# Kernel optimization log

Measured on AMD Instinct MI355X. Metric: run time of the kernel, lower is better.

Reference implementation:

```python
import jax, jax.numpy as jnp
import numpy as np

B, T, D, F, H = 512, 48, 128, 16, 512


def setup_inputs() -> dict:
    key = jax.random.key(0)
    ks = jax.random.split(key, 7)
    return {
        "input": jax.random.normal(ks[0], (B, T, D, F), dtype=jnp.float32),
        "attn_w": jax.random.normal(ks[1], (2 * H + F * T,), dtype=jnp.float32) * 0.02,
        "attn_b": jax.random.normal(ks[2], (1,), dtype=jnp.float32) * 0.02,
        "w_ih": jax.random.normal(ks[3], (4 * H, D * F), dtype=jnp.float32) * 0.02,
        "w_hh": jax.random.normal(ks[4], (4 * H, H), dtype=jnp.float32) * 0.02,
        "b_ih": jax.random.normal(ks[5], (4 * H,), dtype=jnp.float32) * 0.02,
        "b_hh": jax.random.normal(ks[6], (4 * H,), dtype=jnp.float32) * 0.02,
    }


def reference(input, attn_w, attn_b, w_ih, w_hh, b_ih, b_hh):
    Bsz, Ts, Dn, Fn = input.shape
    Hs = w_hh.shape[1]
    # permute(0,2,3,1): [B, T, D, F] -> [B, D, F, T]
    x_perm = jnp.transpose(input, (0, 2, 3, 1))
    x_flat = x_perm.reshape(Bsz, Dn, Fn * Ts)  # [B, D, F*T]
    # encode_attn input is concat(hidden, cell, x); split the weight accordingly
    w_h, w_c, w_x = attn_w[:Hs], attn_w[Hs:2 * Hs], attn_w[2 * Hs:]
    # x contribution to attention logits is constant across steps
    e_x = x_flat @ w_x + attn_b[0]             # [B, D]
    xs = jnp.moveaxis(x_perm, 3, 0)            # [T, B, D, F] (time-major for scan)
    bias = b_ih + b_hh                         # fuse the two LSTM biases

    def step(carry, x_t):
        h, c = carry                           # [B, H] each
        e = e_x + (h @ w_h)[:, None] + (c @ w_c)[:, None]  # [B, D]
        a = jax.nn.softmax(e, axis=-1)
        x_hat = (a[:, :, None] * x_t).reshape(Bsz, Dn * Fn)  # [B, D*F]
        gates = x_hat @ w_ih.T + h @ w_hh.T + bias            # [B, 4H]
        i, f, g, o = jnp.split(gates, 4, axis=-1)  # torch LSTM gate order
        c_new = jax.nn.sigmoid(f) * c + jax.nn.sigmoid(i) * jnp.tanh(g)
        h_new = jax.nn.sigmoid(o) * jnp.tanh(c_new)
        return (h_new, c_new), h_new

    h0 = jnp.zeros((Bsz, Hs), dtype=input.dtype)
    _, hs = jax.lax.scan(step, (h0, h0), xs)   # hs: [T, B, H]
    return jnp.transpose(hs, (1, 0, 2))        # [B, T, H] == hidden_states[:, 1:]
```

## Files before the change

kernel.cpp:

```cpp
#include <hip/hip_runtime.h>

#define B_ 512
#define T_ 48
#define D_ 128
#define F_ 16
#define H_ 512

typedef float f32x4 __attribute__((ext_vector_type(4)));
typedef short s16x8 __attribute__((ext_vector_type(8)));
typedef unsigned short u16x8 __attribute__((ext_vector_type(8)));
typedef unsigned short u16x4 __attribute__((ext_vector_type(4)));
typedef unsigned long long u64;

__device__ __forceinline__ unsigned short f2bf(float x) {
  unsigned u = __float_as_uint(x);
  u += 0x7fffu + ((u >> 16) & 1u);
  return (unsigned short)(u >> 16);
}
__device__ __forceinline__ float bf2f(unsigned short h) {
  return __uint_as_float(((unsigned)h) << 16);
}
__device__ __forceinline__ float sigmoidf_(float x) {
  return 1.f / (1.f + expf(-x));
}

__device__ __forceinline__ void st_sys_u64(u64* p, u64 v) {
  __hip_atomic_store(p, v, __ATOMIC_RELAXED, __HIP_MEMORY_SCOPE_SYSTEM);
}
__device__ __forceinline__ u64 ld_sys_u64(const u64* p) {
  return __hip_atomic_load((u64*)p, __ATOMIC_RELAXED, __HIP_MEMORY_SCOPE_SYSTEM);
}
__device__ __forceinline__ void st_sys_u32(unsigned* p, unsigned v) {
  __hip_atomic_store(p, v, __ATOMIC_RELAXED, __HIP_MEMORY_SCOPE_SYSTEM);
}
__device__ __forceinline__ unsigned ld_sys_u32(const unsigned* p) {
  return __hip_atomic_load((unsigned*)p, __ATOMIC_RELAXED, __HIP_MEMORY_SCOPE_SYSTEM);
}

#define AS1 __attribute__((address_space(1)))
#define AS3 __attribute__((address_space(3)))
__device__ __forceinline__ void g2lds16(const void* g, void* l) {
  __builtin_amdgcn_global_load_lds((const AS1 void*)g, (AS3 void*)l, 16, 0, 0);
}

__global__ __launch_bounds__(256) void k_prep(const float* __restrict__ wih,
                                              const float* __restrict__ whh,
                                              unsigned short* __restrict__ wih_b,
                                              unsigned short* __restrict__ whh_b) {
  long i4 = ((long)blockIdx.x * 256 + threadIdx.x) * 4;
  if (i4 < 4194304) {
    float4 v = *(const float4*)(wih + i4);
    u16x4 o = {f2bf(v.x), f2bf(v.y), f2bf(v.z), f2bf(v.w)};
    *(u16x4*)(wih_b + i4) = o;
  } else {
    long j = i4 - 4194304;
    if (j < 1048576) {
      float4 v = *(const float4*)(whh + j);
      u16x4 o = {f2bf(v.x), f2bf(v.y), f2bf(v.z), f2bf(v.w)};
      *(u16x4*)(whh_b + j) = o;
    }
  }
}

__global__ __launch_bounds__(128) void k_ex(const float* __restrict__ in,
                                            const float* __restrict__ attn_w,
                                            const float* __restrict__ attn_b,
                                            float* __restrict__ a_out) {
  __shared__ float wx[768];
  __shared__ float red[128];
  const int b = blockIdx.x, d = threadIdx.x;
  for (int i = d; i < 768; i += 128) wx[i] = attn_w[1024 + i];
  __syncthreads();
  const float* base = in + (long)b * 98304 + (long)d * 16;
  float acc = 0.f;
  for (int t = 0; t < 48; ++t) {
    const float4* p = (const float4*)(base + (long)t * 2048);
    float4 v0 = p[0], v1 = p[1], v2 = p[2], v3 = p[3];
    acc += v0.x * wx[t]       + v0.y * wx[48 + t]  + v0.z * wx[96 + t]  + v0.w * wx[144 + t];
    acc += v1.x * wx[192 + t] + v1.y * wx[240 + t] + v1.z * wx[288 + t] + v1.w * wx[336 + t];
    acc += v2.x * wx[384 + t] + v2.y * wx[432 + t] + v2.z * wx[480 + t] + v2.w * wx[528 + t];
    acc += v3.x * wx[576 + t] + v3.y * wx[624 + t] + v3.z * wx[672 + t] + v3.w * wx[720 + t];
  }
  acc += attn_b[0];
  red[d] = acc;
  __syncthreads();
  for (int s = 64; s > 0; s >>= 1) {
    if (d < s) red[d] = fmaxf(red[d], red[d + s]);
    __syncthreads();
  }
  float mx = red[0];
  __syncthreads();
  float ex = expf(acc - mx);
  red[d] = ex;
  __syncthreads();
  for (int s = 64; s > 0; s >>= 1) {
    if (d < s) red[d] += red[d + s];
    __syncthreads();
  }
  a_out[b * 128 + d] = ex / red[0];
}

__global__ __launch_bounds__(256) void k_xhat(const float* __restrict__ in,
                                              const float* __restrict__ a,
                                              unsigned short* __restrict__ xh) {
  const int mrow = blockIdx.x;
  const int t = mrow >> 9, b = mrow & 511;
  const int tid = threadIdx.x;
  const int k = tid * 8;
  const int d = k >> 4;
  const int f0 = k & 15;
  const float* src = in + (((long)(b * 48 + t) * 128 + d) * 16 + f0);
  float4 v0 = *(const float4*)src;
  float4 v1 = *(const float4*)(src + 4);
  float s = a[b * 128 + d];
  u16x8 o;
  o[0] = f2bf(v0.x * s); o[1] = f2bf(v0.y * s); o[2] = f2bf(v0.z * s); o[3] = f2bf(v0.w * s);
  o[4] = f2bf(v1.x * s); o[5] = f2bf(v1.y * s); o[6] = f2bf(v1.z * s); o[7] = f2bf(v1.w * s);
  *(u16x8*)(xh + (long)mrow * 2048 + k) = o;
}


#define G_STAGE(ktv, ksv)                                                       \
  do {                                                                          \
    const long ko_ = (long)(ktv) * 64 + (ksv) * 32;                             \
    char* la_ = (char*)SM + ((ktv) & 1) * 32768 + (ksv) * 16384 + ldsw;         \
    g2lds16(Ag + ko_, la_);                                                     \
    g2lds16(Ag + ko_ + 262144, la_ + 8192);                                     \
    g2lds16(Bg + ko_, la_ + 65536);                                             \
    g2lds16(Bg + ko_ + 262144, la_ + 73728);                                    \
  } while (0)

#define G_LDA(bufel, ksv, mh)                                                   \
  do {                                                                          \
    const unsigned short* ab_ = SM + (bufel) + (ksv) * 8192 + aoff0 + (mh) * 2048; \
    af[0] = *(const s16x8*)(ab_);                                               \
    af[1] = *(const s16x8*)(ab_ + 512);                                         \
    af[2] = *(const s16x8*)(ab_ + 1024);                                        \
    af[3] = *(const s16x8*)(ab_ + 1536);                                        \
  } while (0)

#define G_LDB(bufel, ksv)                                                       \
  do {                                                                          \
    const unsigned short* bb_ = SM + (bufel) + (ksv) * 8192 + boff0;            \
    bv[0] = *(const s16x8*)(bb_);                                               \
    bv[1] = *(const s16x8*)(bb_ + 512);                                         \
    bv[2] = *(const s16x8*)(bb_ + 1024);                                        \
    bv[3] = *(const s16x8*)(bb_ + 1536);                                        \
  } while (0)

#define G_BARW()                                                                \
  do {                                                                          \
    __builtin_amdgcn_s_barrier();                                               \
    asm volatile("s_waitcnt lgkmcnt(0)" ::: "memory");                          \
    __builtin_amdgcn_sched_barrier(0);                                          \
  } while (0)

#define G_MMA(mh)                                                               \
  do {                                                                          \
    __builtin_amdgcn_s_setprio(1);                                              \
    _Pragma("unroll") for (int mt_ = 0; mt_ < 4; ++mt_)                         \
        _Pragma("unroll") for (int nt_ = 0; nt_ < 4; ++nt_)                     \
            acc[(mh) * 4 + mt_][nt_] = __builtin_amdgcn_mfma_f32_16x16x32_bf16( \
                af[mt_], bv[nt_], acc[(mh) * 4 + mt_][nt_], 0, 0, 0);           \
    __builtin_amdgcn_s_setprio(0);                                              \
  } while (0)

#define G_GATE(n) asm volatile("s_waitcnt vmcnt(" #n ")" ::: "memory")

__global__ __launch_bounds__(512, 2) void k_gemm(const unsigned short* __restrict__ A,
                                                 const unsigned short* __restrict__ Bw,
                                                 unsigned short* __restrict__ C) {
  __shared__ __align__(16) unsigned short SM[65536];
  const int tid = threadIdx.x;
  const int w = tid >> 6, lane = tid & 63;
  const int q = lane >> 4, l16 = lane & 15;
  const int wm = w >> 2, wn = w & 3;
  const int id = blockIdx.x;
  const int xcd = id & 7, j = id >> 3;
  const long m0 = ((long)xcd * 12 + (j >> 3)) * 256;
  const long n0 = (long)(j & 7) * 256;

  const int srow = w * 16 + (lane >> 2);
  const int csrc = (lane & 3) ^ ((lane >> 2) & 3);
  const unsigned short* Ag = A + (m0 + srow) * 2048 + csrc * 8;
  const unsigned short* Bg = Bw + (n0 + srow) * 2048 + csrc * 8;
  const int ldsw = w * 1024;

  const int psw = (q ^ (l16 & 3)) * 8;
  const int aoff0 = (wm * 128 + l16) * 32 + psw;
  const int boff0 = 32768 + (wn * 64 + l16) * 32 + psw;

  f32x4 acc[8][4];
  const f32x4 zz = {0.f, 0.f, 0.f, 0.f};
#pragma unroll
  for (int i = 0; i < 8; ++i)
#pragma unroll
    for (int j2 = 0; j2 < 4; ++j2) acc[i][j2] = zz;
  s16x8 af[4], bv[4];

  G_STAGE(0, 0);
  G_STAGE(0, 1);
  G_STAGE(1, 0);
  G_GATE(8);
  __builtin_amdgcn_s_barrier();

#pragma unroll 2
  for (int kt = 0; kt < 30; ++kt) {
    const int bufel = (kt & 1) * 16384;
    G_LDB(bufel, 0); G_LDA(bufel, 0, 0);
    G_STAGE(kt + 1, 1);
    G_BARW(); G_MMA(0);
    __builtin_amdgcn_s_barrier();
    G_LDA(bufel, 0, 1);
    G_BARW(); G_MMA(1);
    G_GATE(8);
    __builtin_amdgcn_s_barrier();
    G_LDB(bufel, 1); G_LDA(bufel, 1, 0);
    G_STAGE(kt + 2, 0);
    G_BARW(); G_MMA(0);
    __builtin_amdgcn_s_barrier();
    G_LDA(bufel, 1, 1);
    G_BARW(); G_MMA(1);
    G_GATE(8);
    __builtin_amdgcn_s_barrier();
  }
  {
    G_LDB(0, 0); G_LDA(0, 0, 0);
    G_STAGE(31, 1);
    G_BARW(); G_MMA(0);
    __builtin_amdgcn_s_barrier();
    G_LDA(0, 0, 1);
    G_BARW(); G_MMA(1);
    G_GATE(8);
    __builtin_amdgcn_s_barrier();
    G_LDB(0, 1); G_LDA(0, 1, 0);
    G_BARW(); G_MMA(0);
    __builtin_amdgcn_s_barrier();
    G_LDA(0, 1, 1);
    G_BARW(); G_MMA(1);
    G_GATE(4);
    __builtin_amdgcn_s_barrier();
  }
  {
    G_LDB(16384, 0); G_LDA(16384, 0, 0);
    G_BARW(); G_MMA(0);
    __builtin_amdgcn_s_barrier();
    G_LDA(16384, 0, 1);
    G_BARW(); G_MMA(1);
    G_GATE(0);
    __builtin_amdgcn_s_barrier();
    G_LDB(16384, 1); G_LDA(16384, 1, 0);
    G_BARW(); G_MMA(0);
    __builtin_amdgcn_s_barrier();
    G_LDA(16384, 1, 1);
    G_BARW(); G_MMA(1);
  }

#pragma unroll
  for (int mh = 0; mh < 2; ++mh)
#pragma unroll
    for (int mt = 0; mt < 4; ++mt)
#pragma unroll
      for (int nt = 0; nt < 4; ++nt)
#pragma unroll
        for (int r = 0; r < 4; ++r) {
          long m = m0 + wm * 128 + mh * 64 + mt * 16 + q * 4 + r;
          long n = n0 + wn * 64 + nt * 16 + l16;
          C[m * 2048 + n] = f2bf(acc[mh * 4 + mt][nt][r]);
        }
}

__global__ __launch_bounds__(256, 1) void k_rec(const unsigned short* __restrict__ gx,
                                                const unsigned short* __restrict__ whh_b,
                                                const float* __restrict__ b_ih,
                                                const float* __restrict__ b_hh,
                                                unsigned short* __restrict__ h_buf,
                                                float* __restrict__ out,
                                                unsigned int* __restrict__ bar) {
  __shared__ unsigned short hs[32 * 528];
  __shared__ float gsm[4 * 32 * 36];
  const int tid = threadIdx.x;
  const int wave = tid >> 6, lane = tid & 63;
  const int q = lane >> 4, l16 = lane & 15;
  const int bt = blockIdx.x & 15, g = blockIdx.x >> 4;
  const int b0 = bt * 32;
  const int pm = tid >> 3, pr = (tid & 7) * 4;
  const int srow = tid >> 3, st7 = tid & 7;
  unsigned int* slots = &bar[bt * 16];

  s16x8 wreg[32];
#pragma unroll
  for (int nt = 0; nt < 2; ++nt) {
    const unsigned short* wp = whh_b + (long)(wave * 512 + g * 32 + nt * 16 + l16) * 512 + q * 8;
#pragma unroll
    for (int kk = 0; kk < 16; ++kk)
      wreg[nt * 16 + kk] = *(const s16x8*)(wp + kk * 32);
  }
#pragma unroll
  for (int i = 0; i < 32; ++i) asm volatile("" : "+v"(wreg[i]));

  float bias_[16];
#pragma unroll
  for (int qq = 0; qq < 4; ++qq)
#pragma unroll
    for (int rr = 0; rr < 4; ++rr) {
      int j = qq * 512 + g * 32 + pr + rr;
      bias_[qq * 4 + rr] = b_ih[j] + b_hh[j];
    }
  float creg[4] = {0.f, 0.f, 0.f, 0.f};
  const f32x4 zz = {0.f, 0.f, 0.f, 0.f};

  for (int t = 0; t < 48; ++t) {
    u16x4 gxr[4];
    const unsigned short* gp = gx + ((long)t * 512 + b0 + pm) * 2048 + g * 32 + pr;
#pragma unroll
    for (int qq = 0; qq < 4; ++qq) gxr[qq] = *(const u16x4*)(gp + qq * 512);

    f32x4 acc[2][2] = {{zz, zz}, {zz, zz}};
    if (t > 0) {
      if (wave == 0 && lane < 16) {
        while (ld_sys_u32(&slots[lane]) < (unsigned)t)
          __builtin_amdgcn_s_sleep(1);
      }
      __syncthreads();
      const u64* hp = (const u64*)(h_buf + ((t - 1) & 1) * (512 * 512) + (long)b0 * 512);
      u64 tmp[16];
#pragma unroll
      for (int j = 0; j < 16; ++j)
        tmp[j] = ld_sys_u64(hp + (long)srow * 128 + st7 + 8 * j);
#pragma unroll
      for (int j = 0; j < 16; ++j)
        *(u64*)&hs[srow * 528 + (st7 + 8 * j) * 4] = tmp[j];
      __syncthreads();
#pragma unroll
      for (int kk = 0; kk < 16; ++kk) {
        s16x8 af0 = *(const s16x8*)&hs[l16 * 528 + kk * 32 + q * 8];
        s16x8 af1 = *(const s16x8*)&hs[(16 + l16) * 528 + kk * 32 + q * 8];
        acc[0][0] = __builtin_amdgcn_mfma_f32_16x16x32_bf16(af0, wreg[kk],      acc[0][0], 0, 0, 0);
        acc[0][1] = __builtin_amdgcn_mfma_f32_16x16x32_bf16(af0, wreg[16 + kk], acc[0][1], 0, 0, 0);
        acc[1][0] = __builtin_amdgcn_mfma_f32_16x16x32_bf16(af1, wreg[kk],      acc[1][0], 0, 0, 0);
        acc[1][1] = __builtin_amdgcn_mfma_f32_16x16x32_bf16(af1, wreg[16 + kk], acc[1][1], 0, 0, 0);
      }
    }
#pragma unroll
    for (int mt = 0; mt < 2; ++mt)
#pragma unroll
      for (int nt = 0; nt < 2; ++nt)
        *(f32x4*)&gsm[(wave * 32 + nt * 16 + l16) * 36 + mt * 16 + q * 4] = acc[mt][nt];
    __syncthreads();
    float hval[4];
#pragma unroll
    for (int rr = 0; rr < 4; ++rr) {
      float gv[4];
#pragma unroll
      for (int qq = 0; qq < 4; ++qq)
        gv[qq] = gsm[(qq * 32 + pr + rr) * 36 + pm] + bf2f(gxr[qq][rr]) + bias_[qq * 4 + rr];
      float is = sigmoidf_(gv[0]);
      float fs = sigmoidf_(gv[1]);
      float gt = tanhf(gv[2]);
      float os = sigmoidf_(gv[3]);
      creg[rr] = fs * creg[rr] + is * gt;
      hval[rr] = os * tanhf(creg[rr]);
    }
    u16x4 hb = {f2bf(hval[0]), f2bf(hval[1]), f2bf(hval[2]), f2bf(hval[3])};
    u64 hb8;
    __builtin_memcpy(&hb8, &hb, 8);
    st_sys_u64((u64*)&h_buf[(t & 1) * (512 * 512) + (b0 + pm) * 512 + g * 32 + pr], hb8);
    f32x4 ov = {hval[0], hval[1], hval[2], hval[3]};
    __builtin_nontemporal_store(ov, (f32x4*)&out[(long)(b0 + pm) * (T_ * H_) + (long)t * H_ + g * 32 + pr]);
    __syncthreads();
    if (t < 47 && tid == 0)
      st_sys_u32(&slots[g], (unsigned)(t + 1));
  }
}

extern "C" void kernel_launch(void* const* d_in, const int* in_sizes, int n_in,
                              void* d_out, int out_size, void* d_ws, size_t ws_size,
                              hipStream_t stream) {
  const float* input  = (const float*)d_in[0];
  const float* attn_w = (const float*)d_in[1];
  const float* attn_b = (const float*)d_in[2];
  const float* w_ih   = (const float*)d_in[3];
  const float* w_hh   = (const float*)d_in[4];
  const float* b_ih   = (const float*)d_in[5];
  const float* b_hh   = (const float*)d_in[6];
  float* out = (float*)d_out;

  char* ws = (char*)d_ws;
  unsigned int* bar     = (unsigned int*)ws;
  float* a_ws           = (float*)(ws + 1024);
  unsigned short* h_buf = (unsigned short*)(ws + 263168);
  unsigned short* whh_b = (unsigned short*)(ws + 1311744);
  unsigned short* wih_b = (unsigned short*)(ws + 3408896);
  unsigned short* x_hat = (unsigned short*)(ws + 11797504);
  unsigned short* gxws  = (unsigned short*)(ws + 112460800);

  (void)hipMemsetAsync(d_ws, 0, 1024, stream);
  hipLaunchKernelGGL(k_prep, dim3(5120), dim3(256), 0, stream, w_ih, w_hh, wih_b, whh_b);
  hipLaunchKernelGGL(k_ex, dim3(512), dim3(128), 0, stream, input, attn_w, attn_b, a_ws);
  hipLaunchKernelGGL(k_xhat, dim3(24576), dim3(256), 0, stream, input, a_ws, x_hat);
  hipLaunchKernelGGL(k_gemm, dim3(768), dim3(512), 0, stream, x_hat, wih_b, gxws);
  hipLaunchKernelGGL(k_rec, dim3(256), dim3(256), 0, stream, gxws, whh_b, b_ih, b_hh, h_buf, out, bar);
}
```

Baseline: 757.8 us.

## Restructure GEMM LDS staging to full-K rows and a one-tile-ahead pipeline

```diff
diff --git a/kernel.cpp b/kernel.cpp
--- a/kernel.cpp
+++ b/kernel.cpp
@@ -120,32 +120,33 @@
 }
 
 
-#define G_STAGE(ktv, ksv)                                                       \
-  do {                                                                          \
-    const long ko_ = (long)(ktv) * 64 + (ksv) * 32;                             \
-    char* la_ = (char*)SM + ((ktv) & 1) * 32768 + (ksv) * 16384 + ldsw;         \
+#define G_STAGE(ktv, s)                                                         \
+  do {                                                                          \
+    const long ko_ = (long)(ktv) * 64 + (long)(s) * 262144;                     \
+    char* la_ = (char*)SM + ((ktv) & 1) * 32768 + (s) * 16384 + ldsw;           \
     g2lds16(Ag + ko_, la_);                                                     \
-    g2lds16(Ag + ko_ + 262144, la_ + 8192);                                     \
+    g2lds16(Ag + ko_ + 131072, la_ + 8192);                                     \
     g2lds16(Bg + ko_, la_ + 65536);                                             \
-    g2lds16(Bg + ko_ + 262144, la_ + 73728);                                    \
+    g2lds16(Bg + ko_ + 131072, la_ + 73728);                                    \
   } while (0)
 
 #define G_LDA(bufel, ksv, mh)                                                   \
   do {                                                                          \
-    const unsigned short* ab_ = SM + (bufel) + (ksv) * 8192 + aoff0 + (mh) * 2048; \
+    const unsigned short* ab_ =                                                 \
+        SM + (bufel) + aBase + (mh) * 4096 + (psw ^ ((ksv) * 32));              \
     af[0] = *(const s16x8*)(ab_);                                               \
-    af[1] = *(const s16x8*)(ab_ + 512);                                         \
-    af[2] = *(const s16x8*)(ab_ + 1024);                                        \
-    af[3] = *(const s16x8*)(ab_ + 1536);                                        \
+    af[1] = *(const s16x8*)(ab_ + 1024);                                        \
+    af[2] = *(const s16x8*)(ab_ + 2048);                                        \
+    af[3] = *(const s16x8*)(ab_ + 3072);                                        \
   } while (0)
 
 #define G_LDB(bufel, ksv)                                                       \
   do {                                                                          \
-    const unsigned short* bb_ = SM + (bufel) + (ksv) * 8192 + boff0;            \
+    const unsigned short* bb_ = SM + (bufel) + bBase + (psw ^ ((ksv) * 32));    \
     bv[0] = *(const s16x8*)(bb_);                                               \
-    bv[1] = *(const s16x8*)(bb_ + 512);                                         \
-    bv[2] = *(const s16x8*)(bb_ + 1024);                                        \
-    bv[3] = *(const s16x8*)(bb_ + 1536);                                        \
+    bv[1] = *(const s16x8*)(bb_ + 1024);                                        \
+    bv[2] = *(const s16x8*)(bb_ + 2048);                                        \
+    bv[3] = *(const s16x8*)(bb_ + 3072);                                        \
   } while (0)
 
 #define G_BARW()                                                                \
@@ -180,15 +181,15 @@
   const long m0 = ((long)xcd * 12 + (j >> 3)) * 256;
   const long n0 = (long)(j & 7) * 256;
 
-  const int srow = w * 16 + (lane >> 2);
-  const int csrc = (lane & 3) ^ ((lane >> 2) & 3);
+  const int srow = w * 8 + (lane >> 3);
+  const int csrc = (lane & 7) ^ (lane >> 3);
   const unsigned short* Ag = A + (m0 + srow) * 2048 + csrc * 8;
   const unsigned short* Bg = Bw + (n0 + srow) * 2048 + csrc * 8;
   const int ldsw = w * 1024;
 
-  const int psw = (q ^ (l16 & 3)) * 8;
-  const int aoff0 = (wm * 128 + l16) * 32 + psw;
-  const int boff0 = 32768 + (wn * 64 + l16) * 32 + psw;
+  const int psw = (q ^ (l16 & 7)) * 8;
+  const int aBase = (wm * 128 + l16) * 64;
+  const int bBase = 32768 + (wn * 64 + l16) * 64;
 
   f32x4 acc[8][4];
   const f32x4 zz = {0.f, 0.f, 0.f, 0.f};
@@ -200,45 +201,26 @@
 
   G_STAGE(0, 0);
   G_STAGE(0, 1);
-  G_STAGE(1, 0);
-  G_GATE(8);
+  G_GATE(0);
   __builtin_amdgcn_s_barrier();
 
 #pragma unroll 2
-  for (int kt = 0; kt < 30; ++kt) {
+  for (int kt = 0; kt < 31; ++kt) {
     const int bufel = (kt & 1) * 16384;
     G_LDB(bufel, 0); G_LDA(bufel, 0, 0);
+    G_STAGE(kt + 1, 0);
+    G_BARW(); G_MMA(0);
+    __builtin_amdgcn_s_barrier();
+    G_LDA(bufel, 0, 1);
     G_STAGE(kt + 1, 1);
-    G_BARW(); G_MMA(0);
-    __builtin_amdgcn_s_barrier();
-    G_LDA(bufel, 0, 1);
     G_BARW(); G_MMA(1);
-    G_GATE(8);
     __builtin_amdgcn_s_barrier();
     G_LDB(bufel, 1); G_LDA(bufel, 1, 0);
-    G_STAGE(kt + 2, 0);
     G_BARW(); G_MMA(0);
     __builtin_amdgcn_s_barrier();
     G_LDA(bufel, 1, 1);
     G_BARW(); G_MMA(1);
-    G_GATE(8);
-    __builtin_amdgcn_s_barrier();
-  }
-  {
-    G_LDB(0, 0); G_LDA(0, 0, 0);
-    G_STAGE(31, 1);
-    G_BARW(); G_MMA(0);
-    __builtin_amdgcn_s_barrier();
-    G_LDA(0, 0, 1);
-    G_BARW(); G_MMA(1);
-    G_GATE(8);
-    __builtin_amdgcn_s_barrier();
-    G_LDB(0, 1); G_LDA(0, 1, 0);
-    G_BARW(); G_MMA(0);
-    __builtin_amdgcn_s_barrier();
-    G_LDA(0, 1, 1);
-    G_BARW(); G_MMA(1);
-    G_GATE(4);
+    G_GATE(0);
     __builtin_amdgcn_s_barrier();
   }
   {
@@ -247,7 +229,6 @@
     __builtin_amdgcn_s_barrier();
     G_LDA(16384, 0, 1);
     G_BARW(); G_MMA(1);
-    G_GATE(0);
     __builtin_amdgcn_s_barrier();
     G_LDB(16384, 1); G_LDA(16384, 1, 0);
     G_BARW(); G_MMA(0);
```

Measured after the change: 722.6 us. 1.05x faster.
